# Kernel tuning notes

Measured on AMD Instinct MI355X. Metric: run time of the kernel, lower is better.

Reference implementation:

```python
import jax, jax.numpy as jnp
import numpy as np

B, T, D = 2, 2048, 2048
N_HEADS, N_KV, HEAD_DIM = 16, 8, 128
SOFTCAP = 50.0
BIG_NEG = -2.3819763e38
ROPE_BASE = 10000.0


def apply_rope(x, positions):
    # x: [B, L, N, H], positions: [B, L]
    H = x.shape[-1]
    half = H // 2
    fraction = 2.0 * jnp.arange(half, dtype=jnp.float32) / H
    timescale = ROPE_BASE ** fraction  # [H/2]
    sinusoid = positions.astype(jnp.float32)[:, :, None, None] / timescale[None, None, None, :]  # [B,L,1,H/2]
    sin, cos = jnp.sin(sinusoid), jnp.cos(sinusoid)
    first, second = jnp.split(x, 2, axis=-1)
    out = jnp.concatenate([first * cos - second * sin, second * cos + first * sin], axis=-1)
    return out.astype(x.dtype)


def setup_inputs() -> dict:
    key = jax.random.key(0)
    k1, k2, k3, k4 = jax.random.split(key, 4)
    x = jax.random.normal(k1, (B, T, D), dtype=jnp.float32)
    positions = jnp.broadcast_to(jnp.arange(T, dtype=jnp.int32), (B, T))
    # causal mask [B, 1, T, S]
    attn_mask = jnp.broadcast_to(jnp.tril(jnp.ones((T, T), dtype=bool))[None, None], (B, 1, T, T))
    s = 1.0 / np.sqrt(D)
    w_q = jax.random.normal(k2, (N_HEADS, D, HEAD_DIM), dtype=jnp.float32) * s
    w_kv = jax.random.normal(k3, (2, N_KV, D, HEAD_DIM), dtype=jnp.float32) * s
    w_out = jax.random.normal(k4, (N_HEADS, HEAD_DIM, D), dtype=jnp.float32) * (1.0 / np.sqrt(N_HEADS * HEAD_DIM))
    return {"x": x, "positions": positions, "attn_mask": attn_mask, "w_q": w_q, "w_kv": w_kv, "w_out": w_out}


def reference(x, positions, attn_mask, w_q, w_kv, w_out):
    # projections (GQA branch: num_kv_heads != num_heads)
    q = jnp.einsum('btd,ndh->btnh', x, w_q)            # [B,T,N,H]
    kv = jnp.einsum('bsd,cndh->cbsnh', x, w_kv)        # [2,B,S,K,H]
    k, v = kv[0], kv[1]
    q = apply_rope(q, positions) * (HEAD_DIM ** -0.5)  # rsqrt_head_dim
    k = apply_rope(k, positions)
    G = N_HEADS // N_KV
    q = q.reshape(B, T, N_KV, G, HEAD_DIM)             # B T K G H
    logits = jnp.einsum('btkgh,bskh->bkgts', q, k).astype(jnp.float32)
    logits = jnp.tanh(logits / SOFTCAP) * SOFTCAP
    masked = jnp.where(attn_mask[:, :, None, :, :], logits, BIG_NEG)
    probs = jax.nn.softmax(masked, axis=-1).astype(k.dtype)
    encoded = jnp.einsum('bkgts,bskh->btkgh', probs, v).reshape(B, T, N_HEADS, HEAD_DIM)
    return jnp.einsum('btnh,nhd->btd', encoded, w_out)
```

## Files before the change

kernel.cpp:

```cpp
#include <hip/hip_runtime.h>


typedef unsigned short u16;
typedef __attribute__((ext_vector_type(8))) short short8;
typedef __attribute__((ext_vector_type(4))) float floatx4;

static __device__ __forceinline__ u16 f2b(float f){
  unsigned u = __float_as_uint(f);
  u = (u + 0x7fffu + ((u >> 16) & 1u)) >> 16;
  return (u16)u;
}
static __device__ __forceinline__ float b2f(u16 u){
  return __uint_as_float(((unsigned)u) << 16);
}
static __device__ __forceinline__ void gload16(const u16* g, u16* l){
  __builtin_amdgcn_global_load_lds(
      (const __attribute__((address_space(1))) unsigned int*)g,
      (__attribute__((address_space(3))) unsigned int*)l, 16, 0, 0);
}

static __device__ void tr64(const float* __restrict__ s, u16* __restrict__ d,
                            int sRS, int dRS, float (*t)[65], int tid){
  #pragma unroll
  for(int i = 0; i < 16; i++){
    int idx = tid + 256 * i;
    t[idx >> 6][idx & 63] = s[(long)(idx >> 6) * sRS + (idx & 63)];
  }
  __syncthreads();
  #pragma unroll
  for(int i = 0; i < 16; i++){
    int idx = tid + 256 * i;
    d[(long)(idx >> 6) * dRS + (idx & 63)] = f2b(t[idx & 63][idx >> 6]);
  }
}

__global__ __launch_bounds__(256) void k_prep(
    const float* __restrict__ x, u16* __restrict__ xb,
    const float* __restrict__ wq, u16* __restrict__ wq_t,
    const float* __restrict__ wkv, u16* __restrict__ wkv_t,
    const float* __restrict__ wo, u16* __restrict__ wo_t,
    const int* __restrict__ pos, float* __restrict__ tab){
  __shared__ float t[64][65];
  int blk = blockIdx.x, tid = threadIdx.x;
  if(blk < 8192){
    int i = blk * 256 + tid;
    float4 v = ((const float4*)x)[i];
    ushort4 o = make_ushort4(f2b(v.x), f2b(v.y), f2b(v.z), f2b(v.w));
    ((ushort4*)xb)[i] = o;
  } else if(blk < 9216){
    int q = blk - 8192;
    int bx = q & 1, by = (q >> 1) & 31, bz = q >> 6;
    tr64(wq + (long)bz * 262144 + (long)by * 64 * 128 + bx * 64,
         wq_t + (long)bz * 262144 + (long)bx * 64 * 2048 + by * 64, 128, 2048, t, tid);
  } else if(blk < 10240){
    int q = blk - 9216;
    int bx = q & 1, by = (q >> 1) & 31, bz = q >> 6;
    tr64(wkv + (long)bz * 262144 + (long)by * 64 * 128 + bx * 64,
         wkv_t + (long)bz * 262144 + (long)bx * 64 * 2048 + by * 64, 128, 2048, t, tid);
  } else if(blk < 11264){
    int q = blk - 10240;
    int bx = q & 31, by = q >> 5;
    tr64(wo + (long)by * 64 * 2048 + bx * 64,
         wo_t + (long)bx * 64 * 2048 + by * 64, 2048, 2048, t, tid);
  } else {
    int idx = (blk - 11264) * 256 + tid;
    int row = idx >> 6, h = idx & 63;
    float pf = (float)pos[row];
    float inv = exp2f(-0.20762050593045077f * (float)h);
    float ang = pf * inv;
    tab[(row << 7) + h]      = sinf(ang);
    tab[(row << 7) + 64 + h] = cosf(ang);
  }
}

__global__ __launch_bounds__(256) void k_gemm_qkv(
    const u16* __restrict__ A, const u16* __restrict__ wq_t, const u16* __restrict__ wkv_t,
    const float* __restrict__ tab,
    u16* __restrict__ qb, u16* __restrict__ kb, u16* __restrict__ vtp){
  __shared__ __attribute__((aligned(16))) u16 pool[128 * 132];
  u16* sA = pool;
  u16* sB = pool + 8192;
  int mt = blockIdx.x, nt = blockIdx.y;
  const u16* Bt = (nt < 16) ? (wq_t + (long)nt * 262144)
                            : (wkv_t + (long)(nt - 16) * 262144);
  int tid = threadIdx.x;
  int lane = tid & 63, wave = tid >> 6, l15 = lane & 15, quad = lane >> 4;
  int ro = (wave & 1) * 64, co = (wave >> 1) * 64;
  int xm7 = l15 & 7;
  int srow = tid >> 3;
  int gch  = (tid & 7) ^ (srow & 7);
  const u16* Ag = A  + ((long)(mt * 128) + srow) * 2048 + (gch << 3);
  const u16* Bg = Bt + (long)srow * 2048 + (gch << 3);
  u16* lA = sA + tid * 8;
  u16* lB = sB + tid * 8;
  floatx4 acc[4][4];
  const floatx4 fz = {0.f, 0.f, 0.f, 0.f};
  #pragma unroll
  for(int r = 0; r < 4; r++)
    #pragma unroll
    for(int c = 0; c < 4; c++) acc[r][c] = fz;
  for(int k0 = 0; k0 < 2048; k0 += 64){
    #pragma unroll
    for(int r = 0; r < 4; r++){
      gload16(Ag + (long)r * 65536 + k0, lA + r * 2048);
      gload16(Bg + (long)r * 65536 + k0, lB + r * 2048);
    }
    __syncthreads();
    #pragma unroll
    for(int ks = 0; ks < 2; ks++){
      short8 af[4], bfr[4];
      #pragma unroll
      for(int r = 0; r < 4; r++)
        af[r]  = *(const short8*)(sA + ((ro + r * 16 + l15) << 6) + ((((ks << 2) | quad) ^ xm7) << 3));
      #pragma unroll
      for(int c = 0; c < 4; c++)
        bfr[c] = *(const short8*)(sB + ((co + c * 16 + l15) << 6) + ((((ks << 2) | quad) ^ xm7) << 3));
      #pragma unroll
      for(int r = 0; r < 4; r++)
        #pragma unroll
        for(int c = 0; c < 4; c++)
          acc[r][c] = __builtin_amdgcn_mfma_f32_16x16x32_bf16(af[r], bfr[c], acc[r][c], 0, 0, 0);
    }
    __syncthreads();
  }
  u16* sT = pool;
  #pragma unroll
  for(int r = 0; r < 4; r++)
    #pragma unroll
    for(int c = 0; c < 4; c++){
      int row = ro + r * 16 + quad * 4, col = co + c * 16 + l15;
      #pragma unroll
      for(int j = 0; j < 4; j++) sT[(row + j) * 132 + col] = f2b(acc[r][c][j]);
    }
  __syncthreads();
  int grow0 = mt * 128;
  if(nt < 24){
    float scale = (nt < 16) ? 0.08838834764831845f : 1.0f;
    u16* dst = (nt < 16) ? qb : kb;
    int dS   = (nt < 16) ? 2048 : 1024;
    int dcol = (nt < 16) ? nt * 128 : (nt - 16) * 128;
    #pragma unroll
    for(int it = 0; it < 16; it++){
      int idx = tid + 256 * it;
      int row = idx >> 5, cw = idx & 31;
      int grow = grow0 + row;
      unsigned lo = *(const unsigned*)&sT[row * 132 + 2 * cw];
      unsigned hi = *(const unsigned*)&sT[row * 132 + 64 + 2 * cw];
      float2 sn = *(const float2*)&tab[(grow << 7) + 2 * cw];
      float2 cs = *(const float2*)&tab[(grow << 7) + 64 + 2 * cw];
      float x1a = b2f((u16)lo), x1b = b2f((u16)(lo >> 16));
      float x2a = b2f((u16)hi), x2b = b2f((u16)(hi >> 16));
      float o1a = (x1a * cs.x - x2a * sn.x) * scale;
      float o1b = (x1b * cs.y - x2b * sn.y) * scale;
      float o2a = (x2a * cs.x + x1a * sn.x) * scale;
      float o2b = (x2b * cs.y + x1b * sn.y) * scale;
      unsigned w1 = (unsigned)f2b(o1a) | ((unsigned)f2b(o1b) << 16);
      unsigned w2 = (unsigned)f2b(o2a) | ((unsigned)f2b(o2b) << 16);
      *(unsigned*)&dst[(long)grow * dS + dcol + 2 * cw] = w1;
      *(unsigned*)&dst[(long)grow * dS + dcol + 64 + 2 * cw] = w2;
    }
  } else {
    int b = mt >> 4, kvh = nt - 24;
    u16* vt = vtp + (long)(b * 8 + kvh) * 262144;
    int tcol0 = (mt & 15) * 128;
    int h = tid >> 1, s0 = (tid & 1) * 64;
    #pragma unroll
    for(int i = 0; i < 16; i++){
      int s = s0 + i * 4;
      ushort4 v4 = make_ushort4(sT[(s    ) * 132 + h], sT[(s + 1) * 132 + h],
                                sT[(s + 2) * 132 + h], sT[(s + 3) * 132 + h]);
      *(ushort4*)&vt[(long)h * 2048 + tcol0 + s] = v4;
    }
  }
}

__global__ __launch_bounds__(256) void k_gemm_out(
    const u16* __restrict__ A, const u16* __restrict__ Bt0, float* __restrict__ C){
  __shared__ __attribute__((aligned(16))) u16 sA[128 * 64];
  __shared__ __attribute__((aligned(16))) u16 sB[128 * 64];
  int mt = blockIdx.x, nt = blockIdx.y;
  const u16* Bt = Bt0 + (long)nt * 262144;
  int tid = threadIdx.x;
  int lane = tid & 63, wave = tid >> 6, l15 = lane & 15, quad = lane >> 4;
  int ro = (wave & 1) * 64, co = (wave >> 1) * 64;
  int xm7 = l15 & 7;
  int srow = tid >> 3;
  int gch  = (tid & 7) ^ (srow & 7);
  const u16* Ag = A  + ((long)(mt * 128) + srow) * 2048 + (gch << 3);
  const u16* Bg = Bt + (long)srow * 2048 + (gch << 3);
  u16* lA = sA + tid * 8;
  u16* lB = sB + tid * 8;
  floatx4 acc[4][4];
  const floatx4 fz = {0.f, 0.f, 0.f, 0.f};
  #pragma unroll
  for(int r = 0; r < 4; r++)
    #pragma unroll
    for(int c = 0; c < 4; c++) acc[r][c] = fz;
  for(int k0 = 0; k0 < 2048; k0 += 64){
    #pragma unroll
    for(int r = 0; r < 4; r++){
      gload16(Ag + (long)r * 65536 + k0, lA + r * 2048);
      gload16(Bg + (long)r * 65536 + k0, lB + r * 2048);
    }
    __syncthreads();
    #pragma unroll
    for(int ks = 0; ks < 2; ks++){
      short8 af[4], bfr[4];
      #pragma unroll
      for(int r = 0; r < 4; r++)
        af[r]  = *(const short8*)(sA + ((ro + r * 16 + l15) << 6) + ((((ks << 2) | quad) ^ xm7) << 3));
      #pragma unroll
      for(int c = 0; c < 4; c++)
        bfr[c] = *(const short8*)(sB + ((co + c * 16 + l15) << 6) + ((((ks << 2) | quad) ^ xm7) << 3));
      #pragma unroll
      for(int r = 0; r < 4; r++)
        #pragma unroll
        for(int c = 0; c < 4; c++)
          acc[r][c] = __builtin_amdgcn_mfma_f32_16x16x32_bf16(af[r], bfr[c], acc[r][c], 0, 0, 0);
    }
    __syncthreads();
  }
  long rb0 = (long)mt * 128 + ro + quad * 4;
  #pragma unroll
  for(int r = 0; r < 4; r++)
    #pragma unroll
    for(int c = 0; c < 4; c++){
      int col = nt * 128 + co + c * 16 + l15;
      #pragma unroll
      for(int j = 0; j < 4; j++)
        C[(rb0 + r * 16 + j) * 2048 + col] = acc[r][c][j];
    }
}

__global__ __launch_bounds__(256) void k_flash(
    const u16* __restrict__ qb, const u16* __restrict__ kb,
    const u16* __restrict__ vt, u16* __restrict__ enc){
  __shared__ __attribute__((aligned(16))) u16 sK[2 * 64 * 128];
  __shared__ __attribute__((aligned(16))) u16 sVt[2 * 128 * 64];
  __shared__ __attribute__((aligned(16))) u16 sP[4][16][72];
  int qt = 31 - blockIdx.y;
  int hidx = blockIdx.x;
  int b = hidx >> 4, kv = (hidx >> 1) & 7, g = hidx & 1;
  int tid = threadIdx.x;
  int lane = tid & 63, wave = tid >> 6, l15 = lane & 15, quad = lane >> 4;

  short8 qf[4];
  {
    const u16* qg = qb + ((long)b * 2048 + qt * 64 + wave * 16 + l15) * 2048
                       + (kv * 2 + g) * 128 + quad * 8;
    #pragma unroll
    for(int ks = 0; ks < 4; ks++) qf[ks] = *(const short8*)(qg + ks * 32);
  }

  int krow = tid >> 4;
  int kch  = (tid & 15) ^ krow;
  const u16* Kg = kb + ((long)b * 2048 + krow) * 1024 + kv * 128 + (kch << 3);
  int vrow = tid >> 3;
  int vch  = (tid & 7) ^ (vrow & 7);
  const u16* Vg = vt + ((long)(b * 8 + kv) * 128 + vrow) * 2048 + (vch << 3);
  u16* lK = sK  + tid * 8;
  u16* lV = sVt + tid * 8;
  #pragma unroll
  for(int r = 0; r < 4; r++){
    gload16(Kg + (long)r * 16384, lK + r * 2048);
    gload16(Vg + (long)r * 65536, lV + r * 2048);
  }

  float l_loc[4] = {0.f, 0.f, 0.f, 0.f};
  floatx4 o_acc[8];
  const floatx4 fz = {0.f, 0.f, 0.f, 0.f};
  #pragma unroll
  for(int c = 0; c < 8; c++) o_acc[c] = fz;

  const float c1 = 0.057707801635558536f;
  const float c2 = -144.26950408889634f;
  const float c3 = 72.13475204444817f;

  for(int kt = 0; kt <= qt; kt++){
    int buf = (kt & 1) * 8192;
    __syncthreads();
    if(kt < qt){
      int nb = buf ^ 8192;
      #pragma unroll
      for(int r = 0; r < 4; r++){
        gload16(Kg + (long)(kt + 1) * 65536 + (long)r * 16384, lK + nb + r * 2048);
        gload16(Vg + (kt + 1) * 64 + (long)r * 65536, lV + nb + r * 2048);
      }
    }
    floatx4 s_acc[4];
    #pragma unroll
    for(int c = 0; c < 4; c++) s_acc[c] = fz;
    #pragma unroll
    for(int ks = 0; ks < 4; ks++){
      #pragma unroll
      for(int cb = 0; cb < 4; cb++){
        short8 bk = *(const short8*)(sK + buf + ((cb * 16 + l15) << 7)
                                     + ((((ks << 2) | quad) ^ l15) << 3));
        s_acc[cb] = __builtin_amdgcn_mfma_f32_16x16x32_bf16(qf[ks], bk, s_acc[cb], 0, 0, 0);
      }
    }
    if(kt < qt){
      #pragma unroll
      for(int r = 0; r < 4; r++){
        #pragma unroll
        for(int cb = 0; cb < 4; cb++){
          float s = s_acc[cb][r];
          float u = __builtin_amdgcn_exp2f(c1 * s);
          float d = __builtin_amdgcn_rcpf(u + 1.f);
          float p = __builtin_amdgcn_exp2f(__builtin_fmaf(c2, d, c3));
          l_loc[r] += p;
          sP[wave][quad * 4 + r][cb * 16 + l15] = f2b(p);
        }
      }
    } else {
      int rloc = wave * 16 + quad * 4;
      #pragma unroll
      for(int r = 0; r < 4; r++){
        #pragma unroll
        for(int cb = 0; cb < 4; cb++){
          float s = s_acc[cb][r];
          float u = __builtin_amdgcn_exp2f(c1 * s);
          float d = __builtin_amdgcn_rcpf(u + 1.f);
          float p = __builtin_amdgcn_exp2f(__builtin_fmaf(c2, d, c3));
          if(cb * 16 + l15 > rloc + r) p = 0.f;
          l_loc[r] += p;
          sP[wave][quad * 4 + r][cb * 16 + l15] = f2b(p);
        }
      }
    }
    #pragma unroll
    for(int ks2 = 0; ks2 < 2; ks2++){
      short8 ap = *(const short8*)&sP[wave][l15][ks2 * 32 + quad * 8];
      #pragma unroll
      for(int c = 0; c < 8; c++){
        short8 bv = *(const short8*)(sVt + buf + ((c * 16 + l15) << 6)
                                     + ((((ks2 << 2) | quad) ^ (l15 & 7)) << 3));
        o_acc[c] = __builtin_amdgcn_mfma_f32_16x16x32_bf16(ap, bv, o_acc[c], 0, 0, 0);
      }
    }
  }
  #pragma unroll
  for(int r = 0; r < 4; r++){
    float l = l_loc[r];
    #pragma unroll
    for(int off = 1; off < 16; off <<= 1) l += __shfl_xor(l, off);
    float invl = 1.f / l;
    long rowe = (long)b * 2048 + qt * 64 + wave * 16 + quad * 4 + r;
    #pragma unroll
    for(int c = 0; c < 8; c++)
      enc[rowe * 2048 + (kv * 2 + g) * 128 + c * 16 + l15] = f2b(o_acc[c][r] * invl);
  }
}

extern "C" void kernel_launch(void* const* d_in, const int* in_sizes, int n_in,
                              void* d_out, int out_size, void* d_ws, size_t ws_size,
                              hipStream_t stream){
  const float* x     = (const float*)d_in[0];
  const int*   posi  = (const int*)  d_in[1];
  const float* w_q   = (const float*)d_in[3];
  const float* w_kv  = (const float*)d_in[4];
  const float* w_out = (const float*)d_in[5];
  float* out = (float*)d_out;

  char* w = (char*)d_ws;
  u16* xb     = (u16*)(w);
  u16* wq_t   = (u16*)(w + 16777216);
  u16* wkv_t  = (u16*)(w + 25165824);
  u16* wout_t = (u16*)(w + 33554432);
  u16* q_buf  = (u16*)(w + 41943040);
  u16* k_buf  = (u16*)(w + 58720256);
  u16* v_t    = (u16*)(w + 67108864);
  float* tab  = (float*)(w + 75497472);
  u16* enc    = xb;

  k_prep    <<<12288, 256, 0, stream>>>(x, xb, w_q, wq_t, w_kv, wkv_t, w_out, wout_t, posi, tab);
  k_gemm_qkv<<<dim3(32, 32), 256, 0, stream>>>(xb, wq_t, wkv_t, tab, q_buf, k_buf, v_t);
  k_flash   <<<dim3(32, 32), 256, 0, stream>>>(q_buf, k_buf, v_t, enc);
  k_gemm_out<<<dim3(32, 16), 256, 0, stream>>>(enc, wout_t, out);
}
```

Before: 342.9 us.

## Rewrite QKV GEMM as 256x256 tile with 8 waves and LDS ring pipeline

```diff
diff --git a/kernel.cpp b/kernel.cpp
--- a/kernel.cpp
+++ b/kernel.cpp
@@ -73,106 +73,183 @@
   }
 }
 
-__global__ __launch_bounds__(256) void k_gemm_qkv(
+#define QKV_BAR() do{ __builtin_amdgcn_s_barrier(); \
+                      __builtin_amdgcn_sched_barrier(0); }while(0)
+#define STAGE_A(tt, h) do{ \
+  const u16* s_ = Ag + (tt) * 64 + (h) * 262144; \
+  u16* d_ = ld + ss * 8192; \
+  gload16(s_, d_); gload16(s_ + 131072, d_ + 4096); \
+  ss++; if(ss == 10) ss = 0; }while(0)
+#define STAGE_B(tt, h) do{ \
+  const u16* s_ = Bg + (tt) * 64 + (h) * 262144; \
+  u16* d_ = ld + ss * 8192; \
+  gload16(s_, d_); gload16(s_ + 131072, d_ + 4096); \
+  ss++; if(ss == 10) ss = 0; }while(0)
+
+__global__ __launch_bounds__(512, 2) void k_gemm_qkv(
     const u16* __restrict__ A, const u16* __restrict__ wq_t, const u16* __restrict__ wkv_t,
     const float* __restrict__ tab,
     u16* __restrict__ qb, u16* __restrict__ kb, u16* __restrict__ vtp){
-  __shared__ __attribute__((aligned(16))) u16 pool[128 * 132];
-  u16* sA = pool;
-  u16* sB = pool + 8192;
+  __shared__ __attribute__((aligned(16))) u16 ring[81920];
   int mt = blockIdx.x, nt = blockIdx.y;
-  const u16* Bt = (nt < 16) ? (wq_t + (long)nt * 262144)
-                            : (wkv_t + (long)(nt - 16) * 262144);
+  const u16* Bt = (nt < 8) ? (wq_t + (long)nt * 524288)
+                           : (wkv_t + (long)(nt - 8) * 524288);
   int tid = threadIdx.x;
   int lane = tid & 63, wave = tid >> 6, l15 = lane & 15, quad = lane >> 4;
-  int ro = (wave & 1) * 64, co = (wave >> 1) * 64;
-  int xm7 = l15 & 7;
+  int wr = wave >> 2, wc = wave & 3;
+  int cq0 = quad ^ (l15 & 7), cq1 = cq0 ^ 4;
   int srow = tid >> 3;
   int gch  = (tid & 7) ^ (srow & 7);
-  const u16* Ag = A  + ((long)(mt * 128) + srow) * 2048 + (gch << 3);
+  const u16* Ag = A  + ((long)mt * 256 + srow) * 2048 + (gch << 3);
   const u16* Bg = Bt + (long)srow * 2048 + (gch << 3);
-  u16* lA = sA + tid * 8;
-  u16* lB = sB + tid * 8;
-  floatx4 acc[4][4];
+  u16* ld = ring + tid * 8;
+  int aB = l15 << 6;
+  int bB = ((wc & 1) * 64 + l15) << 6;
+  int sa = wr;
+  int sb = 2 + (wc >> 1);
+  int ss = 0;
+  floatx4 acc[8][4];
   const floatx4 fz = {0.f, 0.f, 0.f, 0.f};
   #pragma unroll
-  for(int r = 0; r < 4; r++)
-    #pragma unroll
-    for(int c = 0; c < 4; c++) acc[r][c] = fz;
-  for(int k0 = 0; k0 < 2048; k0 += 64){
-    #pragma unroll
-    for(int r = 0; r < 4; r++){
-      gload16(Ag + (long)r * 65536 + k0, lA + r * 2048);
-      gload16(Bg + (long)r * 65536 + k0, lB + r * 2048);
+  for(int m = 0; m < 8; m++)
+    #pragma unroll
+    for(int n = 0; n < 4; n++) acc[m][n] = fz;
+
+  STAGE_A(0, 0); STAGE_A(0, 1); STAGE_B(0, 0); STAGE_B(0, 1);
+  STAGE_A(1, 0); STAGE_A(1, 1);
+  asm volatile("s_waitcnt vmcnt(4)" ::: "memory");
+  QKV_BAR();
+
+  #pragma unroll 1
+  for(int t = 0; t < 32; t++){
+    const u16* aS = ring + sa * 8192;
+    const u16* bS = ring + sb * 8192;
+    int tB = (t < 31) ? t + 1 : 31;
+    int tA = (t < 30) ? t + 2 : 31;
+    short8 af[4], bfr[4];
+    #pragma unroll
+    for(int n = 0; n < 4; n++) bfr[n] = *(const short8*)(bS + bB + (n << 10) + (cq0 << 3));
+    #pragma unroll
+    for(int m = 0; m < 4; m++) af[m]  = *(const short8*)(aS + aB + (m << 10) + (cq0 << 3));
+    STAGE_B(tB, 0);
+    QKV_BAR();
+    __builtin_amdgcn_s_setprio(1);
+    #pragma unroll
+    for(int m = 0; m < 4; m++)
+      #pragma unroll
+      for(int n = 0; n < 4; n++)
+        acc[m][n] = __builtin_amdgcn_mfma_f32_16x16x32_bf16(af[m], bfr[n], acc[m][n], 0, 0, 0);
+    __builtin_amdgcn_s_setprio(0);
+    QKV_BAR();
+    #pragma unroll
+    for(int m = 0; m < 4; m++) af[m] = *(const short8*)(aS + aB + 4096 + (m << 10) + (cq0 << 3));
+    STAGE_B(tB, 1);
+    QKV_BAR();
+    __builtin_amdgcn_s_setprio(1);
+    #pragma unroll
+    for(int m = 0; m < 4; m++)
+      #pragma unroll
+      for(int n = 0; n < 4; n++)
+        acc[4 + m][n] = __builtin_amdgcn_mfma_f32_16x16x32_bf16(af[m], bfr[n], acc[4 + m][n], 0, 0, 0);
+    __builtin_amdgcn_s_setprio(0);
+    QKV_BAR();
+    #pragma unroll
+    for(int n = 0; n < 4; n++) bfr[n] = *(const short8*)(bS + bB + (n << 10) + (cq1 << 3));
+    #pragma unroll
+    for(int m = 0; m < 4; m++) af[m]  = *(const short8*)(aS + aB + (m << 10) + (cq1 << 3));
+    STAGE_A(tA, 0);
+    QKV_BAR();
+    __builtin_amdgcn_s_setprio(1);
+    #pragma unroll
+    for(int m = 0; m < 4; m++)
+      #pragma unroll
+      for(int n = 0; n < 4; n++)
+        acc[m][n] = __builtin_amdgcn_mfma_f32_16x16x32_bf16(af[m], bfr[n], acc[m][n], 0, 0, 0);
+    __builtin_amdgcn_s_setprio(0);
+    QKV_BAR();
+    #pragma unroll
+    for(int m = 0; m < 4; m++) af[m] = *(const short8*)(aS + aB + 4096 + (m << 10) + (cq1 << 3));
+    STAGE_A(tA, 1);
+    asm volatile("s_waitcnt vmcnt(4)" ::: "memory");
+    __builtin_amdgcn_sched_barrier(0);
+    QKV_BAR();
+    __builtin_amdgcn_s_setprio(1);
+    #pragma unroll
+    for(int m = 0; m < 4; m++)
+      #pragma unroll
+      for(int n = 0; n < 4; n++)
+        acc[4 + m][n] = __builtin_amdgcn_mfma_f32_16x16x32_bf16(af[m], bfr[n], acc[4 + m][n], 0, 0, 0);
+    __builtin_amdgcn_s_setprio(0);
+    QKV_BAR();
+    sa += 4; if(sa >= 10) sa -= 10;
+    sb += 4; if(sb >= 10) sb -= 10;
+  }
+
+  asm volatile("s_waitcnt vmcnt(0)" ::: "memory");
+  __syncthreads();
+  u16* sT = ring;
+  int grow0 = mt * 256;
+  int hb = wc >> 1, wcl = wc & 1;
+  #pragma unroll 1
+  for(int hh = 0; hh < 2; hh++){
+    if(hb == hh){
+      #pragma unroll
+      for(int m = 0; m < 8; m++){
+        int row = wr * 128 + m * 16 + quad * 4;
+        #pragma unroll
+        for(int n = 0; n < 4; n++){
+          int colh = wcl * 64 + n * 16 + l15;
+          #pragma unroll
+          for(int j = 0; j < 4; j++)
+            sT[(row + j) * 132 + colh] = f2b(acc[m][n][j]);
+        }
+      }
     }
     __syncthreads();
-    #pragma unroll
-    for(int ks = 0; ks < 2; ks++){
-      short8 af[4], bfr[4];
-      #pragma unroll
-      for(int r = 0; r < 4; r++)
-        af[r]  = *(const short8*)(sA + ((ro + r * 16 + l15) << 6) + ((((ks << 2) | quad) ^ xm7) << 3));
-      #pragma unroll
-      for(int c = 0; c < 4; c++)
-        bfr[c] = *(const short8*)(sB + ((co + c * 16 + l15) << 6) + ((((ks << 2) | quad) ^ xm7) << 3));
-      #pragma unroll
-      for(int r = 0; r < 4; r++)
-        #pragma unroll
-        for(int c = 0; c < 4; c++)
-          acc[r][c] = __builtin_amdgcn_mfma_f32_16x16x32_bf16(af[r], bfr[c], acc[r][c], 0, 0, 0);
+    if(nt < 12){
+      float scale = (nt < 8) ? 0.08838834764831845f : 1.0f;
+      u16* dst = (nt < 8) ? qb : kb;
+      int dS   = (nt < 8) ? 2048 : 1024;
+      int dcol = (nt < 8) ? (nt * 2 + hh) * 128 : ((nt - 8) * 2 + hh) * 128;
+      #pragma unroll
+      for(int it = 0; it < 16; it++){
+        int idx = tid + 512 * it;
+        int row = idx >> 5, cw = idx & 31;
+        int grow = grow0 + row;
+        unsigned lo = *(const unsigned*)&sT[row * 132 + 2 * cw];
+        unsigned hi = *(const unsigned*)&sT[row * 132 + 64 + 2 * cw];
+        float2 sn = *(const float2*)&tab[(grow << 7) + 2 * cw];
+        float2 cs = *(const float2*)&tab[(grow << 7) + 64 + 2 * cw];
+        float x1a = b2f((u16)lo), x1b = b2f((u16)(lo >> 16));
+        float x2a = b2f((u16)hi), x2b = b2f((u16)(hi >> 16));
+        float o1a = (x1a * cs.x - x2a * sn.x) * scale;
+        float o1b = (x1b * cs.y - x2b * sn.y) * scale;
+        float o2a = (x2a * cs.x + x1a * sn.x) * scale;
+        float o2b = (x2b * cs.y + x1b * sn.y) * scale;
+        unsigned w1 = (unsigned)f2b(o1a) | ((unsigned)f2b(o1b) << 16);
+        unsigned w2 = (unsigned)f2b(o2a) | ((unsigned)f2b(o2b) << 16);
+        *(unsigned*)&dst[(long)grow * dS + dcol + 2 * cw] = w1;
+        *(unsigned*)&dst[(long)grow * dS + dcol + 64 + 2 * cw] = w2;
+      }
+    } else {
+      int b = mt >> 3, kvh = (nt - 12) * 2 + hh;
+      u16* vt = vtp + (long)(b * 8 + kvh) * 262144;
+      int tcol0 = (mt & 7) * 256;
+      int h = tid >> 2, s0 = (tid & 3) * 64;
+      #pragma unroll
+      for(int i = 0; i < 16; i++){
+        int s = s0 + i * 4;
+        ushort4 v4 = make_ushort4(sT[(s    ) * 132 + h], sT[(s + 1) * 132 + h],
+                                  sT[(s + 2) * 132 + h], sT[(s + 3) * 132 + h]);
+        *(ushort4*)&vt[(long)h * 2048 + tcol0 + s] = v4;
+      }
     }
     __syncthreads();
   }
-  u16* sT = pool;
-  #pragma unroll
-  for(int r = 0; r < 4; r++)
-    #pragma unroll
-    for(int c = 0; c < 4; c++){
-      int row = ro + r * 16 + quad * 4, col = co + c * 16 + l15;
-      #pragma unroll
-      for(int j = 0; j < 4; j++) sT[(row + j) * 132 + col] = f2b(acc[r][c][j]);
-    }
-  __syncthreads();
-  int grow0 = mt * 128;
-  if(nt < 24){
-    float scale = (nt < 16) ? 0.08838834764831845f : 1.0f;
-    u16* dst = (nt < 16) ? qb : kb;
-    int dS   = (nt < 16) ? 2048 : 1024;
-    int dcol = (nt < 16) ? nt * 128 : (nt - 16) * 128;
-    #pragma unroll
-    for(int it = 0; it < 16; it++){
-      int idx = tid + 256 * it;
-      int row = idx >> 5, cw = idx & 31;
-      int grow = grow0 + row;
-      unsigned lo = *(const unsigned*)&sT[row * 132 + 2 * cw];
-      unsigned hi = *(const unsigned*)&sT[row * 132 + 64 + 2 * cw];
-      float2 sn = *(const float2*)&tab[(grow << 7) + 2 * cw];
-      float2 cs = *(const float2*)&tab[(grow << 7) + 64 + 2 * cw];
-      float x1a = b2f((u16)lo), x1b = b2f((u16)(lo >> 16));
-      float x2a = b2f((u16)hi), x2b = b2f((u16)(hi >> 16));
-      float o1a = (x1a * cs.x - x2a * sn.x) * scale;
-      float o1b = (x1b * cs.y - x2b * sn.y) * scale;
-      float o2a = (x2a * cs.x + x1a * sn.x) * scale;
-      float o2b = (x2b * cs.y + x1b * sn.y) * scale;
-      unsigned w1 = (unsigned)f2b(o1a) | ((unsigned)f2b(o1b) << 16);
-      unsigned w2 = (unsigned)f2b(o2a) | ((unsigned)f2b(o2b) << 16);
-      *(unsigned*)&dst[(long)grow * dS + dcol + 2 * cw] = w1;
-      *(unsigned*)&dst[(long)grow * dS + dcol + 64 + 2 * cw] = w2;
-    }
-  } else {
-    int b = mt >> 4, kvh = nt - 24;
-    u16* vt = vtp + (long)(b * 8 + kvh) * 262144;
-    int tcol0 = (mt & 15) * 128;
-    int h = tid >> 1, s0 = (tid & 1) * 64;
-    #pragma unroll
-    for(int i = 0; i < 16; i++){
-      int s = s0 + i * 4;
-      ushort4 v4 = make_ushort4(sT[(s    ) * 132 + h], sT[(s + 1) * 132 + h],
-                                sT[(s + 2) * 132 + h], sT[(s + 3) * 132 + h]);
-      *(ushort4*)&vt[(long)h * 2048 + tcol0 + s] = v4;
-    }
-  }
-}
+}
+#undef STAGE_A
+#undef STAGE_B
+#undef QKV_BAR
 
 __global__ __launch_bounds__(256) void k_gemm_out(
     const u16* __restrict__ A, const u16* __restrict__ Bt0, float* __restrict__ C){
@@ -374,7 +451,7 @@
   u16* enc    = xb;
 
   k_prep    <<<12288, 256, 0, stream>>>(x, xb, w_q, wq_t, w_kv, wkv_t, w_out, wout_t, posi, tab);
-  k_gemm_qkv<<<dim3(32, 32), 256, 0, stream>>>(xb, wq_t, wkv_t, tab, q_buf, k_buf, v_t);
+  k_gemm_qkv<<<dim3(16, 16), 512, 0, stream>>>(xb, wq_t, wkv_t, tab, q_buf, k_buf, v_t);
   k_flash   <<<dim3(32, 32), 256, 0, stream>>>(q_buf, k_buf, v_t, enc);
   k_gemm_out<<<dim3(32, 16), 256, 0, stream>>>(enc, wout_t, out);
 }
```

New measurement: 325.9 us. 1.05x faster.
